# Performance work log

Measured on AMD Instinct MI355X. Metric: run time of the kernel, lower is better.

The kernel has to match this reference:

```python
import jax, jax.numpy as jnp
import numpy as np

SQRT2PI = float(np.sqrt(2.0 * np.pi))
DN = 20          # disperse_number / heat-map side
OUT_CH = 32      # conv out_channels
MINY, MAXY, SD = 0.0, 50.0, 0.3
BN_EPS = 1e-5


def setup_inputs() -> dict:
    key = jax.random.key(0)
    ks = jax.random.split(key, 8)
    N_ATOM, N_ELE, N_NODE = 65536, 16384, 8192
    oe = jax.random.uniform(ks[0], (N_ATOM, 17), dtype=jnp.float32)
    node_ele_idx = jax.random.randint(ks[1], (N_ELE, 4), 0, N_ATOM, dtype=jnp.int64)
    ele_atom_idx = jax.random.randint(ks[2], (N_NODE, 2), 0, N_ELE, dtype=jnp.int64)
    conv_w = jax.random.normal(ks[3], (OUT_CH, 1, 3, 3), dtype=jnp.float32) * 0.1
    conv_b = jnp.zeros((OUT_CH,), jnp.float32)
    bn_gamma = jnp.ones((OUT_CH,), jnp.float32)
    bn_beta = jnp.zeros((OUT_CH,), jnp.float32)
    w1 = jax.random.normal(ks[4], (500, OUT_CH * DN * DN), dtype=jnp.float32) * 0.01
    b1 = jnp.zeros((500,), jnp.float32)
    w2 = jax.random.normal(ks[5], (60, 500), dtype=jnp.float32) * 0.05
    b2 = jnp.zeros((60,), jnp.float32)
    return dict(oe=oe, node_ele_idx=node_ele_idx, ele_atom_idx=ele_atom_idx,
                conv_w=conv_w, conv_b=conv_b, bn_gamma=bn_gamma, bn_beta=bn_beta,
                w1=w1, b1=b1, w2=w2, b2=b2)


def _distribute(rows):
    # rows: (N_node, 17). Gaussian soft histogram onto DN-point grid per row,
    # per-value max-normalization, masked sum over the 17 values, row max-normalization.
    grid = jnp.linspace(MINY, MAXY, DN).astype(rows.dtype)          # (DN,)
    mask = (rows > 0.0) & (rows < 110.0)                            # filter 0 < y < 110
    pdf = jnp.exp(-(grid[None, None, :] - rows[:, :, None]) ** 2 /
                  (2.0 * SD * SD)) / (SQRT2PI * SD)                 # (N, 17, DN)
    m = jnp.max(pdf, axis=-1, keepdims=True)
    pdf = jnp.where(m != 0, pdf / m, pdf)                           # yi / max(yi)
    pdf = pdf * mask[:, :, None]
    s = jnp.sum(pdf, axis=1)                                        # (N, DN)
    smax = jnp.max(s, axis=-1, keepdims=True)
    return jnp.where(smax != 0, s / smax, s)


def reference(oe, node_ele_idx, ele_atom_idx, conv_w, conv_b,
              bn_gamma, bn_beta, w1, b1, w2, b2):
    # merge_idx(oe, node_ele_idx): gather atoms per element, mean-reduce
    g = jnp.mean(oe[node_ele_idx], axis=1)                          # (N_ele, 17)
    g = g / jnp.linalg.norm(g, axis=1, keepdims=True)
    # merge_idx(..., ele_atom_idx, method='sum')
    h = jnp.sum(g[ele_atom_idx], axis=1)                            # (N_node, 17)
    d = _distribute(h)                                              # (N_node, DN)
    # outer-sum heat map: a[n,i,j] = d[n,j], b[n,i,j] = d[n,i]
    x1 = (d[:, None, :] + d[:, :, None])[:, None, :, :]             # (N_node,1,DN,DN)
    x = jax.lax.conv_general_dilated(
        x1, conv_w, window_strides=(1, 1), padding='SAME',
        dimension_numbers=('NCHW', 'OIHW', 'NCHW')) + conv_b[None, :, None, None]
    # Dropout2d is identity in eval mode. BatchNorm2d: training-mode batch stats.
    mu = jnp.mean(x, axis=(0, 2, 3), keepdims=True)
    var = jnp.var(x, axis=(0, 2, 3), keepdims=True)
    xn = (x - mu) / jnp.sqrt(var + BN_EPS)
    x = xn * bn_gamma[None, :, None, None] + bn_beta[None, :, None, None] + x1
    x = x.reshape(x.shape[0], -1)                                   # (N_node, 32*400)
    x = jax.nn.relu(x @ w1.T + b1)
    x = x @ w2.T + b2
    return x.reshape(x.shape[0], 20, 3)
```

## Files before the change

kernel.cpp:

```cpp
#include <hip/hip_runtime.h>
#include <hip/hip_bf16.h>
#include <math.h>

#define NFEAT 17
#define DN 20
#define OCH 32
#define H1 500
#define H2 60

#define DK 4

#define NPB 128
#define NBW 64

#define OFF_D      0
#define OFF_MOMP   32768
#define OFF_MT     33664
#define OFF_PLAIN  34112
#define OFF_M      38112
#define OFF_RS     102112
#define OFF_U4     118112
#define OFF_CST    120112
#define OFF_W2T    120624

__global__ __launch_bounds__(512) void k_main(const float* __restrict__ oe,
                                              const int* __restrict__ nei,
                                              const int* __restrict__ eai,
                                              const float* __restrict__ w2,
                                              const float* __restrict__ convw,
                                              const float* __restrict__ w1,
                                              float* __restrict__ dmat,
                                              float* __restrict__ momp,
                                              float* __restrict__ w2t,
                                              float* __restrict__ MT,
                                              float* __restrict__ plainU2,
                                              float* __restrict__ Mmat,
                                              float* __restrict__ rowsum,
                                              int n_node) {
  __shared__ float smem[9856];
  int tid = threadIdx.x;
  int nbd = (n_node + NPB - 1) / NPB;
  int bx = blockIdx.x;

  if (bx < 2 * H1) {
    int o = bx >> 1, chalf = bx & 1, ch0 = chalf * 16;
    float* sW    = smem;
    float* rowRS = sW + 6720;
    float* rowRW = rowRS + 320;
    float* colCS = rowRW + 960;
    float* colCW = colCS + 320;
    float* swq   = colCW + 960;
    float* swp   = swq + 288;
    if (tid < OCH) {
      int c = tid;
      float w[3][3];
#pragma unroll
      for (int p = 0; p < 3; ++p)
#pragma unroll
        for (int q = 0; q < 3; ++q) w[p][q] = convw[c * 9 + p * 3 + q];
#pragma unroll
      for (int p = 0; p < 3; ++p) {
        swq[(c * 3 + p) * 3 + 0] = w[p][1] + w[p][2];
        swq[(c * 3 + p) * 3 + 1] = w[p][0] + w[p][1] + w[p][2];
        swq[(c * 3 + p) * 3 + 2] = w[p][0] + w[p][1];
      }
#pragma unroll
      for (int q = 0; q < 3; ++q) {
        swp[(c * 3 + q) * 3 + 0] = w[1][q] + w[2][q];
        swp[(c * 3 + q) * 3 + 1] = w[0][q] + w[1][q] + w[2][q];
        swp[(c * 3 + q) * 3 + 2] = w[0][q] + w[1][q];
      }
    }
    __syncthreads();

    const float* wbase = w1 + (size_t)o * (OCH * DN * DN) + ch0 * (DN * DN);
    if (tid < 320) {
      int pair = tid;
      int cl = pair / DN;
      int c = ch0 + cl;
      const float4* r = (const float4*)(wbase + pair * DN);
      float4 v0 = r[0], v1 = r[1], v2 = r[2], v3 = r[3], v4 = r[4];
      float first = v0.x, last = v4.w;
      float rs = v0.x + v0.y + v0.z + v0.w + v1.x + v1.y + v1.z + v1.w +
                 v2.x + v2.y + v2.z + v2.w + v3.x + v3.y + v3.z + v3.w +
                 v4.x + v4.y + v4.z + v4.w;
      float mid = rs - first - last;
#pragma unroll
      for (int p = 0; p < 3; ++p)
        rowRW[p * 320 + pair] = first * swq[(c * 3 + p) * 3 + 0] +
                                mid   * swq[(c * 3 + p) * 3 + 1] +
                                last  * swq[(c * 3 + p) * 3 + 2];
      rowRS[pair] = rs;
      float* dst = &sW[pair * 21];
      dst[0] = v0.x; dst[1] = v0.y; dst[2] = v0.z; dst[3] = v0.w;
      dst[4] = v1.x; dst[5] = v1.y; dst[6] = v1.z; dst[7] = v1.w;
      dst[8] = v2.x; dst[9] = v2.y; dst[10] = v2.z; dst[11] = v2.w;
      dst[12] = v3.x; dst[13] = v3.y; dst[14] = v3.z; dst[15] = v3.w;
      dst[16] = v4.x; dst[17] = v4.y; dst[18] = v4.z; dst[19] = v4.w;
    }
    __syncthreads();
    if (tid < 320) {
      int pair = tid;
      int cl = pair / DN, j = pair - cl * DN;
      int c = ch0 + cl;
      const float* src = &sW[cl * 420 + j];
      float cs = 0.f, first = 0.f, last = 0.f;
#pragma unroll
      for (int i = 0; i < DN; ++i) {
        float vv = src[i * 21];
        cs += vv;
        if (i == 0) first = vv;
        if (i == DN - 1) last = vv;
      }
      float mid = cs - first - last;
#pragma unroll
      for (int q = 0; q < 3; ++q)
        colCW[q * 320 + pair] = first * swp[(c * 3 + q) * 3 + 0] +
                                mid   * swp[(c * 3 + q) * 3 + 1] +
                                last  * swp[(c * 3 + q) * 3 + 2];
      colCS[pair] = cs;
    }
    __syncthreads();
    if (tid < 64) {
      int cl = tid >> 2, a = tid & 3;
      float m = rowRW[320 + cl * 20 + a] + colCW[320 + cl * 20 + a]
              + rowRW[cl * 20 + a + 1]   + colCW[cl * 20 + a + 1];
      if (a > 0) m += rowRW[640 + cl * 20 + a - 1] + colCW[640 + cl * 20 + a - 1];
      Mmat[((size_t)o * OCH + ch0 + cl) * 4 + a] = m;
    } else if (tid >= 64 && tid < 80) {
      int cl = tid - 64;
      float s = 0.f;
#pragma unroll
      for (int i = 0; i < DN; ++i) s += rowRS[cl * 20 + i];
      rowsum[(size_t)o * OCH + ch0 + cl] = s;
    } else if (tid >= 96 && tid < 96 + DK) {
      int a = tid - 96;
      float s = 0.f;
#pragma unroll
      for (int cl = 0; cl < 16; ++cl) s += rowRS[cl * 20 + a] + colCS[cl * 20 + a];
      plainU2[((size_t)o * 2 + chalf) * 4 + a] = s;
    }
    return;
  }

  int rb = bx - 2 * H1;
  if (rb < nbd) {
    float* dls = smem;
    int nl = tid >> 2, t = tid & 3;
    int half = t >> 1;
    int ap = t & 1;
    int n = rb * NPB + nl;

    float a2[NFEAT];
#pragma unroll
    for (int f = 0; f < NFEAT; ++f) a2[f] = 0.f;
    if (n < n_node) {
      int e = eai[(size_t)n * 2 + half];
      int at0 = nei[(size_t)e * 4 + ap * 2 + 0];
      int at1 = nei[(size_t)e * 4 + ap * 2 + 1];
      const float* r0 = oe + (size_t)at0 * NFEAT;
      const float* r1 = oe + (size_t)at1 * NFEAT;
#pragma unroll
      for (int f = 0; f < NFEAT; ++f) a2[f] = r0[f] + r1[f];
    }
    float nrm = 0.f;
    float g[NFEAT];
#pragma unroll
    for (int f = 0; f < NFEAT; ++f) {
      float a4 = (a2[f] + __shfl_xor(a2[f], 1)) * 0.25f;
      g[f] = a4;
      nrm += a4 * a4;
    }
    float inv = 1.0f / sqrtf(nrm);
    float h[NFEAT];
#pragma unroll
    for (int f = 0; f < NFEAT; ++f) {
      float gg = g[f] * inv;
      h[f] = gg + __shfl_xor(gg, 2);
    }

    const float step = 50.0f / 19.0f;
    const float inv2 = 1.0f / (2.0f * 0.3f * 0.3f);
    float s0 = 0.f, s1 = 0.f, s2 = 0.f, s3 = 0.f;
    for (int f = t; f < NFEAT; f += 4) {
      float y = h[f];
      if (!(y > 0.0f && y < 110.0f)) continue;
      float t0 = -y, t1 = step - y, t2 = 2.f * step - y, t3 = 3.f * step - y;
      float e0 = __expf(-t0 * t0 * inv2);
      float e1 = __expf(-t1 * t1 * inv2);
      float e2 = __expf(-t2 * t2 * inv2);
      float e3 = __expf(-t3 * t3 * inv2);
      float mx = fmaxf(fmaxf(e0, e1), fmaxf(e2, e3));
      if (mx > 0.f) {
        float im = 1.0f / mx;
        s0 += e0 * im; s1 += e1 * im; s2 += e2 * im; s3 += e3 * im;
      }
    }
    s0 += __shfl_xor(s0, 1); s1 += __shfl_xor(s1, 1);
    s2 += __shfl_xor(s2, 1); s3 += __shfl_xor(s3, 1);
    s0 += __shfl_xor(s0, 2); s1 += __shfl_xor(s1, 2);
    s2 += __shfl_xor(s2, 2); s3 += __shfl_xor(s3, 2);
    float smax = fmaxf(fmaxf(s0, s1), fmaxf(s2, s3));
    float ism = (smax > 0.f) ? 1.0f / smax : 1.0f;
    if (t == 0) {
      float d0 = s0 * ism, d1 = s1 * ism, d2 = s2 * ism, d3 = s3 * ism;
      dls[nl * 5 + 0] = d0; dls[nl * 5 + 1] = d1;
      dls[nl * 5 + 2] = d2; dls[nl * 5 + 3] = d3;
      if (n < n_node)
        *(float4*)(dmat + (size_t)n * DK) = make_float4(d0, d1, d2, d3);
    }
    __syncthreads();
    if (tid < 14) {
      int u = tid;
      float acc = 0.f;
      if (u < 10) {
        int aa = 0, rem = u;
        while (rem >= DK - aa) { rem -= DK - aa; ++aa; }
        int bb = aa + rem;
        for (int l = 0; l < NPB; ++l) acc += dls[l * 5 + aa] * dls[l * 5 + bb];
      } else {
        int aa = u - 10;
        for (int l = 0; l < NPB; ++l) acc += dls[l * 5 + aa];
      }
      momp[(size_t)u * NBW + rb] = acc;
    }
    return;
  }

  int tb = rb - nbd;
  if (tb < 8) {
    float (*sT)[61] = (float(*)[61])smem;
    int o0 = tb * 64;
    int lo = tid & 63, jr = tid >> 6;
    for (int j = jr; j < H2; j += 8)
      if (o0 + lo < H1) sT[lo][j] = w2[(size_t)j * H1 + o0 + lo];
    __syncthreads();
    int jj = tid & 63, orr = tid >> 6;
    for (int ol = orr; ol < 64; ol += 8) {
      int o = o0 + ol;
      if (o < H1) w2t[(size_t)o * 64 + jj] = (jj < H2) ? sT[ol][jj] : 0.f;
    }
    return;
  }

  {
    float* swqL = smem;
    float* swpL = smem + 288;
    float* MTs  = smem + 576;
    if (tid < OCH) {
      int c = tid;
      float w[3][3];
#pragma unroll
      for (int p = 0; p < 3; ++p)
#pragma unroll
        for (int q = 0; q < 3; ++q) w[p][q] = convw[c * 9 + p * 3 + q];
#pragma unroll
      for (int p = 0; p < 3; ++p) {
        swqL[(c * 3 + p) * 3 + 0] = w[p][1] + w[p][2];
        swqL[(c * 3 + p) * 3 + 1] = w[p][0] + w[p][1] + w[p][2];
        swqL[(c * 3 + p) * 3 + 2] = w[p][0] + w[p][1];
      }
#pragma unroll
      for (int q = 0; q < 3; ++q) {
        swpL[(c * 3 + q) * 3 + 0] = w[1][q] + w[2][q];
        swpL[(c * 3 + q) * 3 + 1] = w[0][q] + w[1][q] + w[2][q];
        swpL[(c * 3 + q) * 3 + 2] = w[0][q] + w[1][q];
      }
    }
    for (int idx = tid; idx < OCH * 14; idx += 512) MTs[idx] = 0.f;
    __syncthreads();
    int c = tid & 31, grp = tid >> 5;
    float wqr[3][3], wpr[3][3];
#pragma unroll
    for (int p = 0; p < 3; ++p)
#pragma unroll
      for (int k = 0; k < 3; ++k) {
        wqr[p][k] = swqL[(c * 3 + p) * 3 + k];
        wpr[p][k] = swpL[(c * 3 + p) * 3 + k];
      }
    float T0 = 0, T1 = 0, T2 = 0, T3 = 0;
    float M0 = 0, M1 = 0, M2 = 0, M3 = 0, M4 = 0, M5 = 0, M6 = 0, M7 = 0, M8 = 0, M9 = 0;
    for (int pos = grp; pos < DN * DN; pos += 16) {
      int i = pos / DN, j = pos - (pos / DN) * DN;
      int icls = (i == 0) ? 0 : ((i == DN - 1) ? 2 : 1);
      int jcls = (j == 0) ? 0 : ((j == DN - 1) ? 2 : 1);
      float t0 = 0, t1 = 0, t2 = 0, t3 = 0;
      int p;
      p = 0 - i + 1; if ((unsigned)p <= 2u) t0 += wqr[p][jcls];
      p = 1 - i + 1; if ((unsigned)p <= 2u) t1 += wqr[p][jcls];
      p = 2 - i + 1; if ((unsigned)p <= 2u) t2 += wqr[p][jcls];
      p = 3 - i + 1; if ((unsigned)p <= 2u) t3 += wqr[p][jcls];
      p = 0 - j + 1; if ((unsigned)p <= 2u) t0 += wpr[p][icls];
      p = 1 - j + 1; if ((unsigned)p <= 2u) t1 += wpr[p][icls];
      p = 2 - j + 1; if ((unsigned)p <= 2u) t2 += wpr[p][icls];
      p = 3 - j + 1; if ((unsigned)p <= 2u) t3 += wpr[p][icls];
      T0 += t0; T1 += t1; T2 += t2; T3 += t3;
      M0 += t0 * t0; M1 += t0 * t1; M2 += t0 * t2; M3 += t0 * t3;
      M4 += t1 * t1; M5 += t1 * t2; M6 += t1 * t3;
      M7 += t2 * t2; M8 += t2 * t3; M9 += t3 * t3;
    }
    atomicAdd(&MTs[c * 14 + 0], T0); atomicAdd(&MTs[c * 14 + 1], T1);
    atomicAdd(&MTs[c * 14 + 2], T2); atomicAdd(&MTs[c * 14 + 3], T3);
    atomicAdd(&MTs[c * 14 + 4], M0); atomicAdd(&MTs[c * 14 + 5], M1);
    atomicAdd(&MTs[c * 14 + 6], M2); atomicAdd(&MTs[c * 14 + 7], M3);
    atomicAdd(&MTs[c * 14 + 8], M4); atomicAdd(&MTs[c * 14 + 9], M5);
    atomicAdd(&MTs[c * 14 + 10], M6); atomicAdd(&MTs[c * 14 + 11], M7);
    atomicAdd(&MTs[c * 14 + 12], M8); atomicAdd(&MTs[c * 14 + 13], M9);
    __syncthreads();
    for (int idx = tid; idx < OCH * 14; idx += 512) MT[idx] = MTs[idx];
  }
}

__global__ __launch_bounds__(512) void k_combine(const float* __restrict__ momp,
                                                 const float* __restrict__ MT,
                                                 const float* __restrict__ convb,
                                                 const float* __restrict__ gamma,
                                                 const float* __restrict__ beta,
                                                 const float* __restrict__ b1,
                                                 const float* __restrict__ plainU2,
                                                 const float* __restrict__ Mmat,
                                                 const float* __restrict__ rowsum,
                                                 int nbd, int n_node,
                                                 float* __restrict__ U4,
                                                 float* __restrict__ Cst) {
  __shared__ float sac[OCH], scc[OCH], phat[10], S4[4], mred[14];
  int tid = threadIdx.x;
  if (tid < 14) {
    float acc = 0.f;
    const float* mp = momp + (size_t)tid * NBW;
    for (int b = 0; b < nbd; ++b) acc += mp[b];
    mred[tid] = acc;
  }
  __syncthreads();
  if (tid < 14) {
    float vv = mred[tid];
    if (tid < 10) {
      int aa = 0, rem = tid;
      while (rem >= DK - aa) { rem -= DK - aa; ++aa; }
      int bb = aa + rem;
      phat[tid] = (aa == bb ? 1.f : 2.f) * vv;
    } else {
      S4[tid - 10] = vv;
    }
  }
  __syncthreads();
  if (tid < OCH) {
    int c = tid;
    const float* mt = MT + c * 14;
    float q2 = mt[0] * S4[0] + mt[1] * S4[1] + mt[2] * S4[2] + mt[3] * S4[3];
    float q1 = 0.f;
#pragma unroll
    for (int u = 0; u < 10; ++u) q1 += mt[4 + u] * phat[u];
    float b_c = convb[c];
    float Nt = (float)n_node * 400.f;
    float S1 = q2 + Nt * b_c;
    float S2 = q1 + 2.f * b_c * q2 + Nt * b_c * b_c;
    float mu = S1 / Nt;
    float var = S2 / Nt - mu * mu;
    float aa = gamma[c] / sqrtf(var + 1e-5f);
    sac[c] = aa;
    scc[c] = aa * (b_c - mu) + beta[c];
  }
  __syncthreads();

  int o0 = blockIdx.x * 63;
  for (int idx = tid; idx < 63 * DK; idx += 512) {
    int ol = idx >> 2, a = idx & 3;
    int o = o0 + ol;
    if (o < H1) {
      float u = plainU2[((size_t)o * 2 + 0) * 4 + a] + plainU2[((size_t)o * 2 + 1) * 4 + a];
      const float* mrow = Mmat + (size_t)o * (OCH * 4) + a;
#pragma unroll
      for (int c = 0; c < OCH; ++c) u += sac[c] * mrow[c * 4];
      U4[o * DK + a] = u;
    }
  }
  if (tid < 63) {
    int o = o0 + tid;
    if (o < H1) {
      float s = b1[o];
      const float* rr = rowsum + (size_t)o * OCH;
#pragma unroll
      for (int c = 0; c < OCH; ++c) s += scc[c] * rr[c];
      Cst[o] = s;
    }
  }
}

#define NTN 16
__global__ __launch_bounds__(256, 4) void k_final(const float* __restrict__ dmat,
                                                  const float* __restrict__ U4,
                                                  const float* __restrict__ Cst,
                                                  const float* __restrict__ w2t,
                                                  const float* __restrict__ b2,
                                                  float* __restrict__ out, int n_node) {
  __shared__ float h1s[H1][20];
  __shared__ float pacc[4][NTN][64];
  int tid = threadIdx.x;
  int n0 = blockIdx.x * NTN;

  {
    int node = tid & 15, kq = tid >> 4;
    float4 d4 = make_float4(0.f, 0.f, 0.f, 0.f);
    if (n0 + node < n_node)
      d4 = *(const float4*)(dmat + (size_t)(n0 + node) * DK);
    for (int k = kq; k < H1; k += 16) {
      float4 u4 = *(const float4*)(U4 + (size_t)k * DK);
      float z = Cst[k] + u4.x * d4.x + u4.y * d4.y + u4.z * d4.z + u4.w * d4.w;
      h1s[k][node] = fmaxf(z, 0.f);
    }
  }
  __syncthreads();

  {
    int w = tid >> 6;
    int lane = tid & 63;
    int q = lane >> 4;
    int og = lane & 15;
    float a0x = 0.f, a0y = 0.f, a0z = 0.f, a0w = 0.f;
    float a1x = 0.f, a1y = 0.f, a1z = 0.f, a1w = 0.f;
    float a2x = 0.f, a2y = 0.f, a2z = 0.f, a2w = 0.f;
    float a3x = 0.f, a3y = 0.f, a3z = 0.f, a3w = 0.f;
    int k0 = w * 125, k1 = k0 + 125;
    for (int k = k0; k < k1; ++k) {
      float4 hv = *(const float4*)&h1s[k][q * 4];
      float4 wv = *(const float4*)(w2t + (size_t)k * 64 + og * 4);
      a0x += hv.x * wv.x; a0y += hv.x * wv.y; a0z += hv.x * wv.z; a0w += hv.x * wv.w;
      a1x += hv.y * wv.x; a1y += hv.y * wv.y; a1z += hv.y * wv.z; a1w += hv.y * wv.w;
      a2x += hv.z * wv.x; a2y += hv.z * wv.y; a2z += hv.z * wv.z; a2w += hv.z * wv.w;
      a3x += hv.w * wv.x; a3y += hv.w * wv.y; a3z += hv.w * wv.z; a3w += hv.w * wv.w;
    }
    *(float4*)&pacc[w][q * 4 + 0][og * 4] = make_float4(a0x, a0y, a0z, a0w);
    *(float4*)&pacc[w][q * 4 + 1][og * 4] = make_float4(a1x, a1y, a1z, a1w);
    *(float4*)&pacc[w][q * 4 + 2][og * 4] = make_float4(a2x, a2y, a2z, a2w);
    *(float4*)&pacc[w][q * 4 + 3][og * 4] = make_float4(a3x, a3y, a3z, a3w);
  }
  __syncthreads();

  for (int idx = tid; idx < NTN * H2; idx += 256) {
    int n = idx / H2, o = idx - n * H2;
    float vv = pacc[0][n][o] + pacc[1][n][o] + pacc[2][n][o] + pacc[3][n][o] + b2[o];
    if (n0 + n < n_node) out[(size_t)(n0 + n) * H2 + o] = vv;
  }
}

extern "C" void kernel_launch(void* const* d_in, const int* in_sizes, int n_in,
                              void* d_out, int out_size, void* d_ws, size_t ws_size,
                              hipStream_t stream) {
  const float* oe    = (const float*)d_in[0];
  const int*   nei   = (const int*)d_in[1];
  const int*   eai   = (const int*)d_in[2];
  const float* convw = (const float*)d_in[3];
  const float* convb = (const float*)d_in[4];
  const float* gamma = (const float*)d_in[5];
  const float* beta  = (const float*)d_in[6];
  const float* w1    = (const float*)d_in[7];
  const float* b1    = (const float*)d_in[8];
  const float* w2    = (const float*)d_in[9];
  const float* b2    = (const float*)d_in[10];
  float* out = (float*)d_out;
  float* ws  = (float*)d_ws;

  int n_node = in_sizes[2] / 2;

  float* dmat    = ws + OFF_D;
  float* momp    = ws + OFF_MOMP;
  float* MT      = ws + OFF_MT;
  float* plainU2 = ws + OFF_PLAIN;
  float* Mmat    = ws + OFF_M;
  float* rowsum  = ws + OFF_RS;
  float* U4      = ws + OFF_U4;
  float* Cst     = ws + OFF_CST;
  float* w2t     = ws + OFF_W2T;

  int nbd = (n_node + NPB - 1) / NPB;
  k_main<<<2 * H1 + nbd + 9, 512, 0, stream>>>(oe, nei, eai, w2, convw, w1,
                                               dmat, momp, w2t, MT,
                                               plainU2, Mmat, rowsum, n_node);
  k_combine<<<8, 512, 0, stream>>>(momp, MT, convb, gamma, beta, b1,
                                   plainU2, Mmat, rowsum, nbd, n_node, U4, Cst);
  k_final<<<(n_node + NTN - 1) / NTN, 256, 0, stream>>>(dmat, U4, Cst, w2t, b2, out, n_node);
}
```

Before: 53.45 us.

## Use two threads per node in gather stage and alias partial sums onto h1 smem

The gather/distribute stage now assigns two threads per node instead of four, so each thread gathers and sums all four atom rows of one element. This removes one shuffle round and doubles the nodes per block (NPB 128 to 256), which halves the block count for that stage. In k_final the partial-accumulator shared array is aliased onto h1s behind an extra barrier, cutting shared memory per block to allow more occupancy. The tradeoff is more serial loads per thread and fewer threads to hide gather latency.

```diff
diff --git a/kernel.cpp b/kernel.cpp
--- a/kernel.cpp
+++ b/kernel.cpp
@@ -10,7 +10,7 @@
 
 #define DK 4
 
-#define NPB 128
+#define NPB 256
 #define NBW 64
 
 #define OFF_D      0
@@ -146,43 +146,40 @@
   int rb = bx - 2 * H1;
   if (rb < nbd) {
     float* dls = smem;
-    int nl = tid >> 2, t = tid & 3;
-    int half = t >> 1;
-    int ap = t & 1;
+    int nl = tid >> 1, half = tid & 1;
     int n = rb * NPB + nl;
 
-    float a2[NFEAT];
-#pragma unroll
-    for (int f = 0; f < NFEAT; ++f) a2[f] = 0.f;
+    float v[NFEAT];
+#pragma unroll
+    for (int f = 0; f < NFEAT; ++f) v[f] = 0.f;
     if (n < n_node) {
       int e = eai[(size_t)n * 2 + half];
-      int at0 = nei[(size_t)e * 4 + ap * 2 + 0];
-      int at1 = nei[(size_t)e * 4 + ap * 2 + 1];
-      const float* r0 = oe + (size_t)at0 * NFEAT;
-      const float* r1 = oe + (size_t)at1 * NFEAT;
-#pragma unroll
-      for (int f = 0; f < NFEAT; ++f) a2[f] = r0[f] + r1[f];
-    }
-    float nrm = 0.f;
-    float g[NFEAT];
-#pragma unroll
-    for (int f = 0; f < NFEAT; ++f) {
-      float a4 = (a2[f] + __shfl_xor(a2[f], 1)) * 0.25f;
-      g[f] = a4;
-      nrm += a4 * a4;
-    }
-    float inv = 1.0f / sqrtf(nrm);
+      float a4[NFEAT];
+#pragma unroll
+      for (int f = 0; f < NFEAT; ++f) a4[f] = 0.f;
+#pragma unroll
+      for (int m = 0; m < 4; ++m) {
+        int at = nei[(size_t)e * 4 + m];
+        const float* row = oe + (size_t)at * NFEAT;
+#pragma unroll
+        for (int f = 0; f < NFEAT; ++f) a4[f] += row[f];
+      }
+      float nrm = 0.f;
+#pragma unroll
+      for (int f = 0; f < NFEAT; ++f) { float t = a4[f] * 0.25f; a4[f] = t; nrm += t * t; }
+      float inv = 1.0f / sqrtf(nrm);
+#pragma unroll
+      for (int f = 0; f < NFEAT; ++f) v[f] = a4[f] * inv;
+    }
     float h[NFEAT];
 #pragma unroll
-    for (int f = 0; f < NFEAT; ++f) {
-      float gg = g[f] * inv;
-      h[f] = gg + __shfl_xor(gg, 2);
-    }
+    for (int f = 0; f < NFEAT; ++f) h[f] = v[f] + __shfl_xor(v[f], 1);
 
     const float step = 50.0f / 19.0f;
     const float inv2 = 1.0f / (2.0f * 0.3f * 0.3f);
     float s0 = 0.f, s1 = 0.f, s2 = 0.f, s3 = 0.f;
-    for (int f = t; f < NFEAT; f += 4) {
+    int f0 = half ? 9 : 0, f1 = half ? NFEAT : 9;
+    for (int f = f0; f < f1; ++f) {
       float y = h[f];
       if (!(y > 0.0f && y < 110.0f)) continue;
       float t0 = -y, t1 = step - y, t2 = 2.f * step - y, t3 = 3.f * step - y;
@@ -198,11 +195,9 @@
     }
     s0 += __shfl_xor(s0, 1); s1 += __shfl_xor(s1, 1);
     s2 += __shfl_xor(s2, 1); s3 += __shfl_xor(s3, 1);
-    s0 += __shfl_xor(s0, 2); s1 += __shfl_xor(s1, 2);
-    s2 += __shfl_xor(s2, 2); s3 += __shfl_xor(s3, 2);
     float smax = fmaxf(fmaxf(s0, s1), fmaxf(s2, s3));
     float ism = (smax > 0.f) ? 1.0f / smax : 1.0f;
-    if (t == 0) {
+    if (half == 0) {
       float d0 = s0 * ism, d1 = s1 * ism, d2 = s2 * ism, d3 = s3 * ism;
       dls[nl * 5 + 0] = d0; dls[nl * 5 + 1] = d1;
       dls[nl * 5 + 2] = d2; dls[nl * 5 + 3] = d3;
@@ -395,7 +390,7 @@
                                                   const float* __restrict__ b2,
                                                   float* __restrict__ out, int n_node) {
   __shared__ float h1s[H1][20];
-  __shared__ float pacc[4][NTN][64];
+  float* pacc = &h1s[0][0];
   int tid = threadIdx.x;
   int n0 = blockIdx.x * NTN;
 
@@ -412,15 +407,15 @@
   }
   __syncthreads();
 
+  int w = tid >> 6;
+  int lane = tid & 63;
+  int q = lane >> 4;
+  int og = lane & 15;
+  float a0x = 0.f, a0y = 0.f, a0z = 0.f, a0w = 0.f;
+  float a1x = 0.f, a1y = 0.f, a1z = 0.f, a1w = 0.f;
+  float a2x = 0.f, a2y = 0.f, a2z = 0.f, a2w = 0.f;
+  float a3x = 0.f, a3y = 0.f, a3z = 0.f, a3w = 0.f;
   {
-    int w = tid >> 6;
-    int lane = tid & 63;
-    int q = lane >> 4;
-    int og = lane & 15;
-    float a0x = 0.f, a0y = 0.f, a0z = 0.f, a0w = 0.f;
-    float a1x = 0.f, a1y = 0.f, a1z = 0.f, a1w = 0.f;
-    float a2x = 0.f, a2y = 0.f, a2z = 0.f, a2w = 0.f;
-    float a3x = 0.f, a3y = 0.f, a3z = 0.f, a3w = 0.f;
     int k0 = w * 125, k1 = k0 + 125;
     for (int k = k0; k < k1; ++k) {
       float4 hv = *(const float4*)&h1s[k][q * 4];
@@ -430,16 +425,19 @@
       a2x += hv.z * wv.x; a2y += hv.z * wv.y; a2z += hv.z * wv.z; a2w += hv.z * wv.w;
       a3x += hv.w * wv.x; a3y += hv.w * wv.y; a3z += hv.w * wv.z; a3w += hv.w * wv.w;
     }
-    *(float4*)&pacc[w][q * 4 + 0][og * 4] = make_float4(a0x, a0y, a0z, a0w);
-    *(float4*)&pacc[w][q * 4 + 1][og * 4] = make_float4(a1x, a1y, a1z, a1w);
-    *(float4*)&pacc[w][q * 4 + 2][og * 4] = make_float4(a2x, a2y, a2z, a2w);
-    *(float4*)&pacc[w][q * 4 + 3][og * 4] = make_float4(a3x, a3y, a3z, a3w);
-  }
+  }
+  __syncthreads();
+
+  *(float4*)&pacc[((w * 16) + q * 4 + 0) * 64 + og * 4] = make_float4(a0x, a0y, a0z, a0w);
+  *(float4*)&pacc[((w * 16) + q * 4 + 1) * 64 + og * 4] = make_float4(a1x, a1y, a1z, a1w);
+  *(float4*)&pacc[((w * 16) + q * 4 + 2) * 64 + og * 4] = make_float4(a2x, a2y, a2z, a2w);
+  *(float4*)&pacc[((w * 16) + q * 4 + 3) * 64 + og * 4] = make_float4(a3x, a3y, a3z, a3w);
   __syncthreads();
 
   for (int idx = tid; idx < NTN * H2; idx += 256) {
     int n = idx / H2, o = idx - n * H2;
-    float vv = pacc[0][n][o] + pacc[1][n][o] + pacc[2][n][o] + pacc[3][n][o] + b2[o];
+    float vv = pacc[(0 * 16 + n) * 64 + o] + pacc[(1 * 16 + n) * 64 + o] +
+               pacc[(2 * 16 + n) * 64 + o] + pacc[(3 * 16 + n) * 64 + o] + b2[o];
     if (n0 + n < n_node) out[(size_t)(n0 + n) * H2 + o] = vv;
   }
 }
```

Result: no change. 53.04 us (-0.8%).
